# Kernel tuning notes

Hardware: AMD Instinct MI355X
Metric: run time of the kernel (lower is better)

## Reference

```python
import jax, jax.numpy as jnp
from jax import lax
import numpy as np

T = 8192          # timesteps (segments)
TOTAL = 1048576   # total ally rows across all timesteps
D_SELF = 128
D_ALLY = 64
H = 20            # h_size_1 == h_size_2
NOUT = 16
LOG_STD_BOUND = 2.0  # Params().log_std_bound (class not shown in source)


def setup_inputs() -> dict:
    key = jax.random.key(0)
    ks = jax.random.split(key, 16)

    def w(k, shape, fan_in):
        b = 1.0 / np.sqrt(fan_in)
        return jax.random.uniform(k, shape, jnp.float32, -b, b)

    # sorted segment ids, every segment in [0,T) guaranteed nonempty
    seg = jnp.sort(jnp.concatenate([
        jnp.arange(T, dtype=jnp.int32),
        jax.random.randint(ks[0], (TOTAL - T,), 0, T, dtype=jnp.int32)]))

    return dict(
        self_input=jax.random.normal(ks[1], (T, D_SELF), jnp.float32),
        ally_input=jax.random.normal(ks[2], (TOTAL, D_ALLY), jnp.float32),
        segment_ids=seg,
        W_self=w(ks[3], (H, D_SELF), D_SELF), b_self=jnp.zeros(H, jnp.float32),
        W_ally=w(ks[4], (H, D_ALLY), D_ALLY), b_ally=jnp.zeros(H, jnp.float32),
        W_cat=w(ks[5], (H, 2 * H), 2 * H), b_cat=jnp.zeros(H, jnp.float32),
        W_ih=w(ks[6], (4 * H, H), H), W_hh=w(ks[7], (4 * H, H), H),
        b_ih=jnp.zeros(4 * H, jnp.float32), b_hh=jnp.zeros(4 * H, jnp.float32),
        W_pfc=w(ks[8], (H, H), H), b_pfc=jnp.zeros(H, jnp.float32),
        W_vfc=w(ks[9], (H, H), H), b_vfc=jnp.zeros(H, jnp.float32),
        W_mu=w(ks[10], (NOUT, H), H), b_mu=jnp.zeros(NOUT, jnp.float32),
        W_ls=w(ks[11], (NOUT, H), H), b_ls=jnp.zeros(NOUT, jnp.float32),
        W_v=w(ks[12], (1, H), H), b_v=jnp.zeros(1, jnp.float32),
        h0=jnp.zeros(H, jnp.float32), c0=jnp.zeros(H, jnp.float32),
    )


def reference(self_input, ally_input, segment_ids, W_self, b_self, W_ally, b_ally,
              W_cat, b_cat, W_ih, W_hh, b_ih, b_hh, W_pfc, b_pfc, W_vfc, b_vfc,
              W_mu, b_mu, W_ls, b_ls, W_v, b_v, h0, c0):
    # per-item Linear+tanh, then ragged mean per timestep (segment mean)
    s = jnp.tanh(self_input @ W_self.T + b_self)                 # [T,H]
    a = jnp.tanh(ally_input @ W_ally.T + b_ally)                 # [TOTAL,H]
    sums = jax.ops.segment_sum(a, segment_ids, num_segments=T)   # [T,H]
    cnts = jax.ops.segment_sum(jnp.ones((a.shape[0], 1), a.dtype),
                               segment_ids, num_segments=T)      # [T,1]
    avg = sums / cnts                                            # [T,H]

    cat_out = jnp.tanh(jnp.concatenate([s, avg], axis=1) @ W_cat.T + b_cat)  # [T,H]

    # single-layer LSTM over T steps (batch=1), torch gate order i,f,g,o
    xg = cat_out @ W_ih.T + (b_ih + b_hh)                        # [T,4H]

    def step(carry, g_x):
        h, c = carry
        g = g_x + W_hh @ h
        i = jax.nn.sigmoid(g[:H])
        f = jax.nn.sigmoid(g[H:2 * H])
        gg = jnp.tanh(g[2 * H:3 * H])
        o = jax.nn.sigmoid(g[3 * H:])
        c = f * c + i * gg
        h = o * jnp.tanh(c)
        return (h, c), h

    _, lstm_out = lax.scan(step, (h0, c0), xg)                   # [T,H]

    x = jnp.tanh(lstm_out @ W_pfc.T + b_pfc)
    mu = jnp.tanh(x @ W_mu.T + b_mu)                             # [T,NOUT]
    log_std = x @ W_ls.T + b_ls                                  # [T,NOUT]
    log_std_out = jnp.exp(jax.nn.relu(log_std) - LOG_STD_BOUND)

    xv = jnp.tanh(cat_out @ W_vfc.T + b_vfc)
    v = xv @ W_v.T + b_v                                         # [T,1]
    return mu, log_std_out, v, log_std
```

## Files before the change

kernel.cpp:

```cpp
#include <hip/hip_runtime.h>
#include <hip/hip_bf16.h>


#define T_STEPS 8192
#define TOTAL_ROWS 1048576
#define DSELF 128
#define DALLY 64
#define HS 20
#define NOUT 16
#define L2E 1.44269504088896340736f

typedef float v2f __attribute__((ext_vector_type(2)));

__device__ __forceinline__ float rcp_f(float x) { return __builtin_amdgcn_rcpf(x); }
__device__ __forceinline__ float sigm_f(float x) { return rcp_f(1.0f + __expf(-x)); }
__device__ __forceinline__ float tanh_f(float x) { return fmaf(2.0f, sigm_f(2.0f * x), -1.0f); }

__device__ __forceinline__ v2f pk_fma(v2f acc, v2f w, v2f h) {
  asm("v_pk_fma_f32 %0, %1, %2, %0" : "+v"(acc) : "v"(w), "s"(h));
  return acc;
}
__device__ __forceinline__ v2f pk_add(v2f a, v2f b) {
  v2f d;
  asm("v_pk_add_f32 %0, %1, %2" : "=v"(d) : "v"(a), "v"(b));
  return d;
}

__global__ __launch_bounds__(64) void k_segmean(
    const float* __restrict__ ally, const int* __restrict__ seg,
    const float* __restrict__ W_ally, const float* __restrict__ b_ally,
    float* __restrict__ avg) {
  __shared__ float tile[64][DALLY + 2];
  __shared__ float red[64][HS + 1];
  const int lane = threadIdx.x;
  const int s = blockIdx.x;
  int r0;
  {
    int lo = 0, hi = TOTAL_ROWS;
    while (lo < hi) { int mid = (lo + hi) >> 1; if (seg[mid] < s) lo = mid + 1; else hi = mid; }
    r0 = lo;
  }
  int r1;
  if (s == T_STEPS - 1) {
    r1 = TOTAL_ROWS;
  } else {
    int lo = r0, hi = TOTAL_ROWS;
    const int sp = s + 1;
    while (lo < hi) { int mid = (lo + hi) >> 1; if (seg[mid] < sp) lo = mid + 1; else hi = mid; }
    r1 = lo;
  }
  float acc[HS];
#pragma unroll
  for (int h = 0; h < HS; ++h) acc[h] = 0.0f;
  for (int base = r0; base < r1; base += 64) {
    const int m = min(64, r1 - base);
    __syncthreads();
    for (int idx = lane; idx < m * 16; idx += 64) {
      const int rr = idx >> 4, cc = (idx & 15) << 2;
      const float4 v = *reinterpret_cast<const float4*>(
          ally + (size_t)(base + rr) * DALLY + cc);
      *reinterpret_cast<float2*>(&tile[rr][cc])     = make_float2(v.x, v.y);
      *reinterpret_cast<float2*>(&tile[rr][cc + 2]) = make_float2(v.z, v.w);
    }
    __syncthreads();
    if (lane < m) {
      float dot[HS];
#pragma unroll
      for (int h = 0; h < HS; ++h) dot[h] = b_ally[h];
#pragma unroll
      for (int j = 0; j < DALLY; j += 4) {
        const float2 xa = *reinterpret_cast<const float2*>(&tile[lane][j]);
        const float2 xb = *reinterpret_cast<const float2*>(&tile[lane][j + 2]);
#pragma unroll
        for (int h = 0; h < HS; ++h) {
          const float4 w = *reinterpret_cast<const float4*>(&W_ally[h * DALLY + j]);
          dot[h] = fmaf(xa.x, w.x, dot[h]);
          dot[h] = fmaf(xa.y, w.y, dot[h]);
          dot[h] = fmaf(xb.x, w.z, dot[h]);
          dot[h] = fmaf(xb.y, w.w, dot[h]);
        }
      }
#pragma unroll
      for (int h = 0; h < HS; ++h) acc[h] += tanh_f(dot[h]);
    }
  }
#pragma unroll
  for (int h = 0; h < HS; ++h) red[lane][h] = acc[h];
  __syncthreads();
  if (lane < HS) {
    float t = 0.0f;
    for (int l = 0; l < 64; ++l) t += red[l][lane];
    avg[(size_t)s * HS + lane] = t / (float)(r1 - r0);
  }
}

__global__ __launch_bounds__(128) void k_feats(
    const float* __restrict__ self_in, const float* __restrict__ avg,
    const float* __restrict__ W_self, const float* __restrict__ b_self,
    const float* __restrict__ W_cat, const float* __restrict__ b_cat,
    const float* __restrict__ W_ih, const float* __restrict__ b_ih,
    const float* __restrict__ b_hh,
    const float* __restrict__ W_vfc, const float* __restrict__ b_vfc,
    const float* __restrict__ W_v, const float* __restrict__ b_v,
    float* __restrict__ xg, float* __restrict__ v_out) {
  __shared__ float s_ws[HS * DSELF];
  __shared__ float s_bs[HS];
  __shared__ float s_wc[HS * 2 * HS];
  __shared__ float s_bc[HS];
  __shared__ float s_wih[4 * HS * HS];
  __shared__ float s_bih[4 * HS];
  __shared__ float s_wv[HS * HS];
  __shared__ float s_bv[HS];
  __shared__ float s_wvv[HS];
  __shared__ float s_bvs;
  const int tid = threadIdx.x;
  for (int i = tid; i < HS * DSELF; i += 128) s_ws[i] = W_self[i];
  for (int i = tid; i < HS * 2 * HS; i += 128) s_wc[i] = W_cat[i];
  for (int i = tid; i < 4 * HS * HS; i += 128) {
    const float sc = (i >= 800 && i < 1200) ? (2.0f * L2E) : L2E;
    s_wih[i] = W_ih[i] * sc;
  }
  for (int i = tid; i < HS * HS; i += 128) s_wv[i] = W_vfc[i];
  if (tid < HS) {
    s_bs[tid] = b_self[tid]; s_bc[tid] = b_cat[tid];
    s_bv[tid] = b_vfc[tid];  s_wvv[tid] = W_v[tid];
  }
  if (tid < 4 * HS) {
    const float sc = (tid >= 40 && tid < 60) ? (2.0f * L2E) : L2E;
    s_bih[tid] = (b_ih[tid] + b_hh[tid]) * sc;
  }
  if (tid == 0) s_bvs = b_v[0];
  __syncthreads();

  const int t = blockIdx.x * 128 + tid;
  const float* srow = self_in + (size_t)t * DSELF;
  float acc[HS];
#pragma unroll
  for (int h = 0; h < HS; ++h) acc[h] = s_bs[h];
  for (int j = 0; j < DSELF / 4; ++j) {
    const float4 x = *reinterpret_cast<const float4*>(srow + j * 4);
#pragma unroll
    for (int h = 0; h < HS; ++h) {
      const float4 w = *reinterpret_cast<const float4*>(&s_ws[h * DSELF + j * 4]);
      acc[h] = fmaf(x.x, w.x, acc[h]);
      acc[h] = fmaf(x.y, w.y, acc[h]);
      acc[h] = fmaf(x.z, w.z, acc[h]);
      acc[h] = fmaf(x.w, w.w, acc[h]);
    }
  }
  float sv[HS], av[HS];
#pragma unroll
  for (int h = 0; h < HS; ++h) sv[h] = tanh_f(acc[h]);
  {
    const float4* ap = reinterpret_cast<const float4*>(avg + (size_t)t * HS);
#pragma unroll
    for (int q = 0; q < HS / 4; ++q) {
      const float4 a4 = ap[q];
      av[q * 4 + 0] = a4.x; av[q * 4 + 1] = a4.y;
      av[q * 4 + 2] = a4.z; av[q * 4 + 3] = a4.w;
    }
  }
  float cat[HS];
#pragma unroll
  for (int h = 0; h < HS; ++h) {
    float a = s_bc[h];
#pragma unroll
    for (int j = 0; j < HS; ++j) a = fmaf(sv[j], s_wc[h * 2 * HS + j], a);
#pragma unroll
    for (int j = 0; j < HS; ++j) a = fmaf(av[j], s_wc[h * 2 * HS + HS + j], a);
    cat[h] = tanh_f(a);
  }
#pragma unroll 2
  for (int jj = 0; jj < 4 * HS; jj += 4) {
    float a0 = s_bih[jj], a1 = s_bih[jj + 1], a2 = s_bih[jj + 2], a3 = s_bih[jj + 3];
#pragma unroll
    for (int k = 0; k < HS; ++k) {
      const float cv = cat[k];
      a0 = fmaf(cv, s_wih[(jj + 0) * HS + k], a0);
      a1 = fmaf(cv, s_wih[(jj + 1) * HS + k], a1);
      a2 = fmaf(cv, s_wih[(jj + 2) * HS + k], a2);
      a3 = fmaf(cv, s_wih[(jj + 3) * HS + k], a3);
    }
    float4 o4; o4.x = a0; o4.y = a1; o4.z = a2; o4.w = a3;
    *reinterpret_cast<float4*>(&xg[(size_t)t * 80 + jj]) = o4;
  }
  float vacc = s_bvs;
#pragma unroll
  for (int h = 0; h < HS; ++h) {
    float a = s_bv[h];
#pragma unroll
    for (int k = 0; k < HS; ++k) a = fmaf(cat[k], s_wv[h * HS + k], a);
    vacc = fmaf(tanh_f(a), s_wvv[h], vacc);
  }
  v_out[t] = vacc;
}

#define LSTM_STEP(X1, X2, K)                                                  \
  do {                                                                        \
    v2f pA = {(X1), 0.0f}, pB = {0.0f, 0.0f};                                 \
    v2f qA = {(X2), 0.0f}, qB = {0.0f, 0.0f};                                 \
    _Pragma("unroll") for (int j = 0; j < 10; j += 2) {                       \
      const v2f h2a = {hs[2 * j],     hs[2 * j + 1]};                         \
      const v2f h2b = {hs[2 * j + 2], hs[2 * j + 3]};                         \
      pA = pk_fma(pA, wa2[j],     h2a);                                       \
      qA = pk_fma(qA, wb2[j],     h2a);                                       \
      pB = pk_fma(pB, wa2[j + 1], h2b);                                       \
      qB = pk_fma(qB, wb2[j + 1], h2b);                                       \
    }                                                                         \
    pA = pk_add(pA, pB);                                                      \
    qA = pk_add(qA, qB);                                                      \
    const float a1 = pA.x + pA.y;                                             \
    const float a2 = qA.x + qA.y;                                             \
    (X1) = px1[(K + 8) * 80];                                                 \
    (X2) = px2[(K + 8) * 80];                                                 \
    const float e1 = __builtin_amdgcn_exp2f(-a1);                             \
    const float e2 = __builtin_amdgcn_exp2f(-a2);                             \
    const float d1 = 1.0f + e1;                                               \
    const float d2 = 1.0f + e2;                                               \
    const float R  = rcp_f(d1 * d2);                                          \
    const float n  = fmaf(Bn, e2, An);               \
    const float m  = fmaf(2.0f, e1, 2.0f);                   \
    const float P1 = n * R;                                     \
    const float P2 = m * R;                                    \
    auto rfp = __builtin_amdgcn_permlane32_swap(                              \
        __float_as_uint(P1), __float_as_uint(P1), false, false);              \
    auto rop = __builtin_amdgcn_permlane32_swap(                              \
        __float_as_uint(P2), __float_as_uint(P2), false, false);              \
    const float fp  = __uint_as_float(rfp[1]);               \
    const float op2 = __uint_as_float(rop[1]);             \
    cs = fmaf(fp, cs, P1);                                   \
    const float ho = -0.5f * op2;                               \
    const float ec = __builtin_amdgcn_exp2f(-cs);                             \
    const float uc = rcp_f(1.0f + ec);                           \
    const float hn = fmaf(op2, uc, ho);                      \
    if (lane < HS) hp[(K)*HS] = hn;                                           \
    const unsigned hu = __float_as_uint(hn);                                  \
    _Pragma("unroll") for (int j = 0; j < HS; ++j)                            \
        hs[j] = __uint_as_float(__builtin_amdgcn_readlane(hu, j));            \
  } while (0)

__global__ __launch_bounds__(64) void k_lstm(
    const float* __restrict__ xg, const float* __restrict__ Whh,
    const float* __restrict__ h0, const float* __restrict__ c0,
    float* __restrict__ hout) {
  const int lane = threadIdx.x;
  const int kk = lane & 31;
  const int kc = kk < HS ? kk : HS - 1;
  const int r1 = kc + ((lane >= 32) ? HS : 0);
  const int r2 = r1 + 2 * HS;

  const float An = (lane < 32) ? 2.0f * L2E : 1.0f;
  const float Bn = (lane < 32) ? -2.0f * L2E : 1.0f;
  const float s2v = (lane < 32) ? 2.0f * L2E : L2E;

  v2f wa2[10], wb2[10];
  {
    const v2f* ra = reinterpret_cast<const v2f*>(Whh + (size_t)r1 * HS);
    const v2f* rb = reinterpret_cast<const v2f*>(Whh + (size_t)r2 * HS);
#pragma unroll
    for (int j = 0; j < 10; ++j) {
      v2f a = ra[j], b = rb[j];
      a.x *= L2E; a.y *= L2E;
      b.x *= s2v; b.y *= s2v;
      wa2[j] = a; wb2[j] = b;
    }
  }

  float hs[HS];
#pragma unroll
  for (int j = 0; j < HS; ++j) hs[j] = h0[j];
  float cs = c0[kc] * (2.0f * L2E);

  const float* px1 = xg + r1;
  const float* px2 = xg + r2;
  float x10 = px1[0 * 80], x20 = px2[0 * 80];
  float x11 = px1[1 * 80], x21 = px2[1 * 80];
  float x12 = px1[2 * 80], x22 = px2[2 * 80];
  float x13 = px1[3 * 80], x23 = px2[3 * 80];
  float x14 = px1[4 * 80], x24 = px2[4 * 80];
  float x15 = px1[5 * 80], x25 = px2[5 * 80];
  float x16 = px1[6 * 80], x26 = px2[6 * 80];
  float x17 = px1[7 * 80], x27 = px2[7 * 80];
  float* hp = hout + lane;

  for (int t = 0; t < T_STEPS; t += 8) {
    LSTM_STEP(x10, x20, 0);
    LSTM_STEP(x11, x21, 1);
    LSTM_STEP(x12, x22, 2);
    LSTM_STEP(x13, x23, 3);
    LSTM_STEP(x14, x24, 4);
    LSTM_STEP(x15, x25, 5);
    LSTM_STEP(x16, x26, 6);
    LSTM_STEP(x17, x27, 7);
    px1 += 8 * 80; px2 += 8 * 80; hp += 8 * HS;
  }
}

__global__ __launch_bounds__(128) void k_heads(
    const float* __restrict__ hbuf,
    const float* __restrict__ W_pfc, const float* __restrict__ b_pfc,
    const float* __restrict__ W_mu, const float* __restrict__ b_mu,
    const float* __restrict__ W_ls, const float* __restrict__ b_ls,
    float* __restrict__ mu_out, float* __restrict__ lso_out,
    float* __restrict__ ls_out) {
  __shared__ float wp[HS * HS], bp[HS], wm[NOUT * HS], bm[NOUT], wl[NOUT * HS], bl[NOUT];
  const int tid = threadIdx.x;
  for (int i = tid; i < HS * HS; i += 128) wp[i] = W_pfc[i];
  for (int i = tid; i < NOUT * HS; i += 128) { wm[i] = W_mu[i]; wl[i] = W_ls[i]; }
  if (tid < HS) bp[tid] = b_pfc[tid];
  if (tid < NOUT) { bm[tid] = b_mu[tid]; bl[tid] = b_ls[tid]; }
  __syncthreads();
  const int t = blockIdx.x * 128 + tid;
  float hr[HS];
  {
    const float4* hp4 = reinterpret_cast<const float4*>(hbuf + (size_t)t * HS);
#pragma unroll
    for (int q = 0; q < HS / 4; ++q) {
      const float4 h4 = hp4[q];
      hr[q * 4 + 0] = h4.x; hr[q * 4 + 1] = h4.y;
      hr[q * 4 + 2] = h4.z; hr[q * 4 + 3] = h4.w;
    }
  }
  float x[HS];
#pragma unroll
  for (int h = 0; h < HS; ++h) {
    float a = bp[h];
#pragma unroll
    for (int k = 0; k < HS; ++k) a = fmaf(hr[k], wp[h * HS + k], a);
    x[h] = tanh_f(a);
  }
  float4* mo4 = reinterpret_cast<float4*>(mu_out + (size_t)t * NOUT);
  float4* lo4 = reinterpret_cast<float4*>(lso_out + (size_t)t * NOUT);
  float4* lb4 = reinterpret_cast<float4*>(ls_out + (size_t)t * NOUT);
#pragma unroll
  for (int m = 0; m < NOUT; m += 4) {
    float4 mu4, lsb4, lso4;
    float am[4], bm_[4];
#pragma unroll
    for (int q = 0; q < 4; ++q) { am[q] = bm[m + q]; bm_[q] = bl[m + q]; }
#pragma unroll
    for (int k = 0; k < HS; ++k) {
      const float xv = x[k];
#pragma unroll
      for (int q = 0; q < 4; ++q) {
        am[q]  = fmaf(xv, wm[(m + q) * HS + k], am[q]);
        bm_[q] = fmaf(xv, wl[(m + q) * HS + k], bm_[q]);
      }
    }
    mu4.x = tanh_f(am[0]); mu4.y = tanh_f(am[1]);
    mu4.z = tanh_f(am[2]); mu4.w = tanh_f(am[3]);
    lsb4.x = bm_[0]; lsb4.y = bm_[1]; lsb4.z = bm_[2]; lsb4.w = bm_[3];
    lso4.x = __expf(fmaxf(bm_[0], 0.0f) - 2.0f);
    lso4.y = __expf(fmaxf(bm_[1], 0.0f) - 2.0f);
    lso4.z = __expf(fmaxf(bm_[2], 0.0f) - 2.0f);
    lso4.w = __expf(fmaxf(bm_[3], 0.0f) - 2.0f);
    mo4[m / 4] = mu4; lb4[m / 4] = lsb4; lo4[m / 4] = lso4;
  }
}

extern "C" void kernel_launch(void* const* d_in, const int* in_sizes, int n_in,
                              void* d_out, int out_size, void* d_ws, size_t ws_size,
                              hipStream_t stream) {
  const float* self_in = (const float*)d_in[0];
  const float* ally_in = (const float*)d_in[1];
  const int*   seg     = (const int*)d_in[2];
  const float* W_self  = (const float*)d_in[3];
  const float* b_self  = (const float*)d_in[4];
  const float* W_ally  = (const float*)d_in[5];
  const float* b_ally  = (const float*)d_in[6];
  const float* W_cat   = (const float*)d_in[7];
  const float* b_cat   = (const float*)d_in[8];
  const float* W_ih    = (const float*)d_in[9];
  const float* W_hh    = (const float*)d_in[10];
  const float* b_ih    = (const float*)d_in[11];
  const float* b_hh    = (const float*)d_in[12];
  const float* W_pfc   = (const float*)d_in[13];
  const float* b_pfc   = (const float*)d_in[14];
  const float* W_vfc   = (const float*)d_in[15];
  const float* b_vfc   = (const float*)d_in[16];
  const float* W_mu    = (const float*)d_in[17];
  const float* b_mu    = (const float*)d_in[18];
  const float* W_ls    = (const float*)d_in[19];
  const float* b_ls    = (const float*)d_in[20];
  const float* W_v     = (const float*)d_in[21];
  const float* b_v     = (const float*)d_in[22];
  const float* h0      = (const float*)d_in[23];
  const float* c0      = (const float*)d_in[24];
  float* out = (float*)d_out;

  char* ws = (char*)d_ws;
  float* avg   = (float*)(ws + 36864);
  float* xg    = (float*)(ws + 692224);
  float* hbuf  = (float*)(ws + 3313664);

  float* mu_out  = out;
  float* lso_out = out + 131072;
  float* v_out   = out + 262144;
  float* ls_out  = out + 270336;

  k_segmean<<<T_STEPS, 64, 0, stream>>>(ally_in, seg, W_ally, b_ally, avg);
  k_feats<<<T_STEPS / 128, 128, 0, stream>>>(self_in, avg, W_self, b_self,
                                             W_cat, b_cat, W_ih, b_ih, b_hh,
                                             W_vfc, b_vfc, W_v, b_v, xg, v_out);
  k_lstm<<<1, 64, 0, stream>>>(xg, W_hh, h0, c0, hbuf);
  k_heads<<<T_STEPS / 128, 128, 0, stream>>>(hbuf, W_pfc, b_pfc, W_mu, b_mu,
                                             W_ls, b_ls, mu_out, lso_out, ls_out);
}
```

Before: 1.570 ms.

## Interleave xg gate layout for paired LSTM loads and trim step arithmetic

k_feats now writes the input-gate preactivations interleaved, so the two gate values each LSTM lane needs sit next to each other. The serial LSTM kernel can then fetch them with one 8-byte load per step instead of two scalar loads, and the sigmoid output algebra loses a couple of operations. The point is to shorten the latency-bound recurrent loop. Block sizes of the feats and heads kernels also go from 128 to 256, which halves their block count to 32 on a large GPU and may lower parallelism.

```diff
diff --git a/kernel.cpp b/kernel.cpp
--- a/kernel.cpp
+++ b/kernel.cpp
@@ -94,7 +94,7 @@
   }
 }
 
-__global__ __launch_bounds__(128) void k_feats(
+__global__ __launch_bounds__(256) void k_feats(
     const float* __restrict__ self_in, const float* __restrict__ avg,
     const float* __restrict__ W_self, const float* __restrict__ b_self,
     const float* __restrict__ W_cat, const float* __restrict__ b_cat,
@@ -114,13 +114,13 @@
   __shared__ float s_wvv[HS];
   __shared__ float s_bvs;
   const int tid = threadIdx.x;
-  for (int i = tid; i < HS * DSELF; i += 128) s_ws[i] = W_self[i];
-  for (int i = tid; i < HS * 2 * HS; i += 128) s_wc[i] = W_cat[i];
-  for (int i = tid; i < 4 * HS * HS; i += 128) {
+  for (int i = tid; i < HS * DSELF; i += 256) s_ws[i] = W_self[i];
+  for (int i = tid; i < HS * 2 * HS; i += 256) s_wc[i] = W_cat[i];
+  for (int i = tid; i < 4 * HS * HS; i += 256) {
     const float sc = (i >= 800 && i < 1200) ? (2.0f * L2E) : L2E;
     s_wih[i] = W_ih[i] * sc;
   }
-  for (int i = tid; i < HS * HS; i += 128) s_wv[i] = W_vfc[i];
+  for (int i = tid; i < HS * HS; i += 256) s_wv[i] = W_vfc[i];
   if (tid < HS) {
     s_bs[tid] = b_self[tid]; s_bc[tid] = b_cat[tid];
     s_bv[tid] = b_vfc[tid];  s_wvv[tid] = W_v[tid];
@@ -132,7 +132,7 @@
   if (tid == 0) s_bvs = b_v[0];
   __syncthreads();
 
-  const int t = blockIdx.x * 128 + tid;
+  const int t = blockIdx.x * 256 + tid;
   const float* srow = self_in + (size_t)t * DSELF;
   float acc[HS];
 #pragma unroll
@@ -171,18 +171,19 @@
     cat[h] = tanh_f(a);
   }
 #pragma unroll 2
-  for (int jj = 0; jj < 4 * HS; jj += 4) {
-    float a0 = s_bih[jj], a1 = s_bih[jj + 1], a2 = s_bih[jj + 2], a3 = s_bih[jj + 3];
+  for (int j = 0; j < 40; j += 2) {
+    float a0 = s_bih[j],      a1 = s_bih[j + 40];
+    float a2 = s_bih[j + 1],  a3 = s_bih[j + 41];
 #pragma unroll
     for (int k = 0; k < HS; ++k) {
       const float cv = cat[k];
-      a0 = fmaf(cv, s_wih[(jj + 0) * HS + k], a0);
-      a1 = fmaf(cv, s_wih[(jj + 1) * HS + k], a1);
-      a2 = fmaf(cv, s_wih[(jj + 2) * HS + k], a2);
-      a3 = fmaf(cv, s_wih[(jj + 3) * HS + k], a3);
+      a0 = fmaf(cv, s_wih[(j + 0)  * HS + k], a0);
+      a1 = fmaf(cv, s_wih[(j + 40) * HS + k], a1);
+      a2 = fmaf(cv, s_wih[(j + 1)  * HS + k], a2);
+      a3 = fmaf(cv, s_wih[(j + 41) * HS + k], a3);
     }
     float4 o4; o4.x = a0; o4.y = a1; o4.z = a2; o4.w = a3;
-    *reinterpret_cast<float4*>(&xg[(size_t)t * 80 + jj]) = o4;
+    *reinterpret_cast<float4*>(&xg[(size_t)t * 80 + 2 * j]) = o4;
   }
   float vacc = s_bvs;
 #pragma unroll
@@ -195,10 +196,10 @@
   v_out[t] = vacc;
 }
 
-#define LSTM_STEP(X1, X2, K)                                                  \
+#define LSTM_STEP(X, K)                                                       \
   do {                                                                        \
-    v2f pA = {(X1), 0.0f}, pB = {0.0f, 0.0f};                                 \
-    v2f qA = {(X2), 0.0f}, qB = {0.0f, 0.0f};                                 \
+    v2f pA = {(X).x, 0.0f}, pB = {0.0f, 0.0f};                                \
+    v2f qA = {(X).y, 0.0f}, qB = {0.0f, 0.0f};                                \
     _Pragma("unroll") for (int j = 0; j < 10; j += 2) {                       \
       const v2f h2a = {hs[2 * j],     hs[2 * j + 1]};                         \
       const v2f h2b = {hs[2 * j + 2], hs[2 * j + 3]};                         \
@@ -211,28 +212,26 @@
     qA = pk_add(qA, qB);                                                      \
     const float a1 = pA.x + pA.y;                                             \
     const float a2 = qA.x + qA.y;                                             \
-    (X1) = px1[(K + 8) * 80];                                                 \
-    (X2) = px2[(K + 8) * 80];                                                 \
+    (X) = pxp[(K + 8) * 40];                                                  \
     const float e1 = __builtin_amdgcn_exp2f(-a1);                             \
     const float e2 = __builtin_amdgcn_exp2f(-a2);                             \
     const float d1 = 1.0f + e1;                                               \
     const float d2 = 1.0f + e2;                                               \
     const float R  = rcp_f(d1 * d2);                                          \
-    const float n  = fmaf(Bn, e2, An);               \
-    const float m  = fmaf(2.0f, e1, 2.0f);                   \
+    const float n  = fmaf(Bn, e2, An);                   \
     const float P1 = n * R;                                     \
-    const float P2 = m * R;                                    \
+    const float P2 = d1 * R;                               \
     auto rfp = __builtin_amdgcn_permlane32_swap(                              \
         __float_as_uint(P1), __float_as_uint(P1), false, false);              \
     auto rop = __builtin_amdgcn_permlane32_swap(                              \
         __float_as_uint(P2), __float_as_uint(P2), false, false);              \
-    const float fp  = __uint_as_float(rfp[1]);               \
-    const float op2 = __uint_as_float(rop[1]);             \
+    const float fp = __uint_as_float(rfp[1]);                \
+    const float op = __uint_as_float(rop[1]);                \
     cs = fmaf(fp, cs, P1);                                   \
-    const float ho = -0.5f * op2;                               \
+    const float op2 = op + op;                                  \
     const float ec = __builtin_amdgcn_exp2f(-cs);                             \
     const float uc = rcp_f(1.0f + ec);                           \
-    const float hn = fmaf(op2, uc, ho);                      \
+    const float hn = fmaf(op2, uc, -op);                     \
     if (lane < HS) hp[(K)*HS] = hn;                                           \
     const unsigned hu = __float_as_uint(hn);                                  \
     _Pragma("unroll") for (int j = 0; j < HS; ++j)                            \
@@ -248,6 +247,7 @@
   const int kc = kk < HS ? kk : HS - 1;
   const int r1 = kc + ((lane >= 32) ? HS : 0);
   const int r2 = r1 + 2 * HS;
+  const int idx = ((lane >= 32) ? HS : 0) + kc;
 
   const float An = (lane < 32) ? 2.0f * L2E : 1.0f;
   const float Bn = (lane < 32) ? -2.0f * L2E : 1.0f;
@@ -271,32 +271,25 @@
   for (int j = 0; j < HS; ++j) hs[j] = h0[j];
   float cs = c0[kc] * (2.0f * L2E);
 
-  const float* px1 = xg + r1;
-  const float* px2 = xg + r2;
-  float x10 = px1[0 * 80], x20 = px2[0 * 80];
-  float x11 = px1[1 * 80], x21 = px2[1 * 80];
-  float x12 = px1[2 * 80], x22 = px2[2 * 80];
-  float x13 = px1[3 * 80], x23 = px2[3 * 80];
-  float x14 = px1[4 * 80], x24 = px2[4 * 80];
-  float x15 = px1[5 * 80], x25 = px2[5 * 80];
-  float x16 = px1[6 * 80], x26 = px2[6 * 80];
-  float x17 = px1[7 * 80], x27 = px2[7 * 80];
+  const v2f* pxp = reinterpret_cast<const v2f*>(xg) + idx;
+  v2f X0 = pxp[0 * 40], X1 = pxp[1 * 40], X2 = pxp[2 * 40], X3 = pxp[3 * 40];
+  v2f X4 = pxp[4 * 40], X5 = pxp[5 * 40], X6 = pxp[6 * 40], X7 = pxp[7 * 40];
   float* hp = hout + lane;
 
   for (int t = 0; t < T_STEPS; t += 8) {
-    LSTM_STEP(x10, x20, 0);
-    LSTM_STEP(x11, x21, 1);
-    LSTM_STEP(x12, x22, 2);
-    LSTM_STEP(x13, x23, 3);
-    LSTM_STEP(x14, x24, 4);
-    LSTM_STEP(x15, x25, 5);
-    LSTM_STEP(x16, x26, 6);
-    LSTM_STEP(x17, x27, 7);
-    px1 += 8 * 80; px2 += 8 * 80; hp += 8 * HS;
-  }
-}
-
-__global__ __launch_bounds__(128) void k_heads(
+    LSTM_STEP(X0, 0);
+    LSTM_STEP(X1, 1);
+    LSTM_STEP(X2, 2);
+    LSTM_STEP(X3, 3);
+    LSTM_STEP(X4, 4);
+    LSTM_STEP(X5, 5);
+    LSTM_STEP(X6, 6);
+    LSTM_STEP(X7, 7);
+    pxp += 8 * 40; hp += 8 * HS;
+  }
+}
+
+__global__ __launch_bounds__(256) void k_heads(
     const float* __restrict__ hbuf,
     const float* __restrict__ W_pfc, const float* __restrict__ b_pfc,
     const float* __restrict__ W_mu, const float* __restrict__ b_mu,
@@ -305,12 +298,12 @@
     float* __restrict__ ls_out) {
   __shared__ float wp[HS * HS], bp[HS], wm[NOUT * HS], bm[NOUT], wl[NOUT * HS], bl[NOUT];
   const int tid = threadIdx.x;
-  for (int i = tid; i < HS * HS; i += 128) wp[i] = W_pfc[i];
-  for (int i = tid; i < NOUT * HS; i += 128) { wm[i] = W_mu[i]; wl[i] = W_ls[i]; }
+  for (int i = tid; i < HS * HS; i += 256) wp[i] = W_pfc[i];
+  for (int i = tid; i < NOUT * HS; i += 256) { wm[i] = W_mu[i]; wl[i] = W_ls[i]; }
   if (tid < HS) bp[tid] = b_pfc[tid];
   if (tid < NOUT) { bm[tid] = b_mu[tid]; bl[tid] = b_ls[tid]; }
   __syncthreads();
-  const int t = blockIdx.x * 128 + tid;
+  const int t = blockIdx.x * 256 + tid;
   float hr[HS];
   {
     const float4* hp4 = reinterpret_cast<const float4*>(hbuf + (size_t)t * HS);
@@ -399,10 +392,10 @@
   float* ls_out  = out + 270336;
 
   k_segmean<<<T_STEPS, 64, 0, stream>>>(ally_in, seg, W_ally, b_ally, avg);
-  k_feats<<<T_STEPS / 128, 128, 0, stream>>>(self_in, avg, W_self, b_self,
+  k_feats<<<T_STEPS / 256, 256, 0, stream>>>(self_in, avg, W_self, b_self,
                                              W_cat, b_cat, W_ih, b_ih, b_hh,
                                              W_vfc, b_vfc, W_v, b_v, xg, v_out);
   k_lstm<<<1, 64, 0, stream>>>(xg, W_hh, h0, c0, hbuf);
-  k_heads<<<T_STEPS / 128, 128, 0, stream>>>(hbuf, W_pfc, b_pfc, W_mu, b_mu,
+  k_heads<<<T_STEPS / 256, 256, 0, stream>>>(hbuf, W_pfc, b_pfc, W_mu, b_mu,
                                              W_ls, b_ls, mu_out, lso_out, ls_out);
 }
```

Result: slower. 1.618 ms (+3.1%).
